# Kernel tuning notes

Hardware: AMD Instinct MI355X
Metric: run time of the kernel (lower is better)

## Reference

```python
import jax, jax.numpy as jnp
import numpy as np

N = 100_000   # nodes
E = 3_200_000 # edges
F = 512       # input features
H = 64        # hidden
C = 64        # classes
K = 10        # APPNP propagation steps
ALPHA = 0.1


def setup_inputs() -> dict:
    key = jax.random.key(0)
    k0, k1, k2, k3 = jax.random.split(key, 4)
    x = jax.random.normal(k0, (N, F), dtype=jnp.float32)
    W1 = jax.random.normal(k1, (H, F), dtype=jnp.float32) / np.float32(np.sqrt(F))
    b1 = jnp.zeros((H,), dtype=jnp.float32)
    W2 = jax.random.normal(k2, (C, H), dtype=jnp.float32) / np.float32(np.sqrt(H))
    b2 = jnp.zeros((C,), dtype=jnp.float32)
    edge_index = jax.random.randint(k3, (2, E), 0, N, dtype=jnp.int64)
    return {"x": x, "W1": W1, "b1": b1, "W2": W2, "b2": b2, "edge_index": edge_index}


def reference(x, W1, b1, W2, b2, edge_index):
    src = edge_index[0]  # message source (x_j)
    dst = edge_index[1]  # aggregation target
    # GCN normalization with self-loops: deg_i = 1 + sum of incoming edge weights
    deg = jax.ops.segment_sum(jnp.ones((E,), x.dtype), dst, num_segments=N) + 1.0
    dinv = jax.lax.rsqrt(deg)
    norm = dinv[src] * dinv[dst]      # per-edge coefficient
    self_w = dinv * dinv              # self-loop coefficient d_i^{-1}

    # MLP (dropout is identity in eval mode)
    h = jax.nn.relu(x @ W1.T + b1)
    h = h @ W2.T + b2                 # [N, C]

    # APPNP: z <- (1-alpha) * A_hat z + alpha * h, repeated K times
    z = h
    for _ in range(K):
        agg = jax.ops.segment_sum(norm[:, None] * z[src], dst, num_segments=N)
        agg = agg + self_w[:, None] * z
        z = (1.0 - ALPHA) * agg + ALPHA * h

    return jax.nn.log_softmax(z, axis=1)
```

## Files before the change

kernel.cpp:

```cpp
#include <hip/hip_runtime.h>
#include <hip/hip_bf16.h>

#define N_NODES 100000
#define N_EDGES 3200000
#define F_IN    512
#define H_DIM   64
#define C_DIM   64
#define K_STEPS 10
#define ALPHA   0.1f
#define RSTRIDE 96
#define NBINS   256
#define BINW    391
#define SLOTS   16384
#define EPB     4096

typedef __attribute__((ext_vector_type(8))) short bf16x8;
typedef __attribute__((ext_vector_type(4))) float f32x4;

__device__ __forceinline__ float bf2f(ushort u) {
    union { unsigned int i; float f; } c; c.i = ((unsigned int)u) << 16; return c.f;
}
__device__ __forceinline__ ushort f2bf(float f) {
    union { float f; unsigned int i; } c; c.f = f;
    unsigned int lsb = (c.i >> 16) & 1u;
    unsigned int r = c.i + 0x7fffu + lsb;
    return (ushort)(r >> 16);
}
__device__ __forceinline__ uint cvtpk(float a, float b) {
    uint r;
    asm("v_cvt_pk_bf16_f32 %0, %1, %2" : "=v"(r) : "v"(a), "v"(b));
    return r;
}

__global__ __launch_bounds__(256) void binA_kernel(
    const int* __restrict__ src, const int* __restrict__ dst,
    int* __restrict__ gcursor, uint* __restrict__ staging, int e)
{
    __shared__ int cnt[NBINS], sbase[NBINS], loff[NBINS], gbase[NBINS];
    __shared__ int wsum[4];
    __shared__ uint recs[EPB];
    __shared__ uchar binarr[EPB];
    int t = threadIdx.x;
    cnt[t] = 0; loff[t] = 0;
    __syncthreads();

    int blk = blockIdx.x * EPB;
    int nhere = e - blk; nhere = (nhere < EPB) ? nhere : EPB;

    #pragma unroll
    for (int j = 0; j < EPB / 256; ++j) {
        int i = blk + j * 256 + t;
        if (i < e) atomicAdd(&cnt[dst[i] / BINW], 1);
    }
    __syncthreads();

    int lane = t & 63, w = t >> 6;
    int v = cnt[t], incl = v;
    #pragma unroll
    for (int off = 1; off < 64; off <<= 1) {
        int u = __shfl_up(incl, off);
        if (lane >= off) incl += u;
    }
    if (lane == 63) wsum[w] = incl;
    __syncthreads();
    int woff = 0;
    #pragma unroll
    for (int j = 0; j < 4; ++j) woff += (j < w) ? wsum[j] : 0;
    sbase[t] = woff + (incl - v);
    gbase[t] = (v > 0) ? atomicAdd(&gcursor[t], v) : 0;
    __syncthreads();

    #pragma unroll
    for (int j = 0; j < EPB / 256; ++j) {
        int i = blk + j * 256 + t;
        if (i < e) {
            int ss = src[i], dd = dst[i];
            int b = dd / BINW;
            int dl = dd - b * BINW;
            int idx = sbase[b] + atomicAdd(&loff[b], 1);
            recs[idx] = (uint)ss | ((uint)dl << 17);
            binarr[idx] = (uchar)b;
        }
    }
    __syncthreads();

    #pragma unroll
    for (int j = 0; j < EPB / 256; ++j) {
        int idx = j * 256 + t;
        if (idx < nhere) {
            int b = binarr[idx];
            int gp = gbase[b] + (idx - sbase[b]);
            if (gp < SLOTS)
                staging[(size_t)b * SLOTS + gp] = recs[idx];
        }
    }
}

__global__ __launch_bounds__(256) void binB_kernel(
    const int* __restrict__ gcursor, const uint* __restrict__ staging,
    int* __restrict__ deg, float* __restrict__ dinv, float* __restrict__ selfc,
    int* __restrict__ esrc, int n)
{
    __shared__ int dloc[BINW];
    int b = blockIdx.x, t = threadIdx.x;
    for (int i = t; i < BINW; i += 256) dloc[i] = 0;
    __syncthreads();

    int cnt = gcursor[b];
    cnt = (cnt < SLOTS) ? cnt : SLOTS;
    const uint* st = staging + (size_t)b * SLOTS;
    int nb = b * BINW;

    int j = t;
    for (; j + 768 < cnt; j += 1024) {
        uint p0 = st[j], p1 = st[j + 256], p2 = st[j + 512], p3 = st[j + 768];
        int d0 = p0 >> 17, d1 = p1 >> 17, d2 = p2 >> 17, d3 = p3 >> 17;
        int q0 = atomicAdd(&dloc[d0], 1);
        int q1 = atomicAdd(&dloc[d1], 1);
        int q2 = atomicAdd(&dloc[d2], 1);
        int q3 = atomicAdd(&dloc[d3], 1);
        if (q0 < RSTRIDE) esrc[(size_t)(nb + d0) * RSTRIDE + q0] = (int)(p0 & 0x1FFFFu);
        if (q1 < RSTRIDE) esrc[(size_t)(nb + d1) * RSTRIDE + q1] = (int)(p1 & 0x1FFFFu);
        if (q2 < RSTRIDE) esrc[(size_t)(nb + d2) * RSTRIDE + q2] = (int)(p2 & 0x1FFFFu);
        if (q3 < RSTRIDE) esrc[(size_t)(nb + d3) * RSTRIDE + q3] = (int)(p3 & 0x1FFFFu);
    }
    for (; j < cnt; j += 256) {
        uint p = st[j];
        int d = p >> 17;
        int q = atomicAdd(&dloc[d], 1);
        if (q < RSTRIDE) esrc[(size_t)(nb + d) * RSTRIDE + q] = (int)(p & 0x1FFFFu);
    }
    __syncthreads();
    for (int i = t; i < BINW; i += 256) {
        int node = nb + i;
        if (node < n) {
            int dg = dloc[i];
            deg[node] = dg;
            float d = rsqrtf((float)dg + 1.0f);
            dinv[node]  = d;
            selfc[node] = (1.0f - ALPHA) * d * d;
        }
    }
}

__global__ void cvt_w_kernel(const float* __restrict__ W1, const float* __restrict__ W2,
                             ushort* __restrict__ w1bf, ushort* __restrict__ w2bf) {
    int i = blockIdx.x * blockDim.x + threadIdx.x;
    if (i < 64 * 512) w1bf[i] = f2bf(W1[i]);
    if (i < 64 * 64)  w2bf[i] = f2bf(W2[i]);
}

__global__ __launch_bounds__(64, 4) void mlp_mfma_kernel(
    const float* __restrict__ x, const ushort* __restrict__ w1bf, const float* __restrict__ b1,
    const ushort* __restrict__ w2bf, const float* __restrict__ b2, const float* __restrict__ dinv,
    ushort* __restrict__ y0, ushort* __restrict__ g, int n)
{
    __shared__ ushort h1s[4096];
    __shared__ float  b1s[64], b2s[64];

    int t = threadIdx.x;
    b1s[t] = b1[t];
    b2s[t] = b2[t];
    __syncthreads();

    int lr = t & 15;
    int lk = t >> 4;
    int rowbase = blockIdx.x * 64;

    f32x4 acc[4][4] = {};
    for (int kk = 0; kk < 16; ++kk) {
        int k0 = kk * 32 + lk * 8;
        bf16x8 a[4];
        #pragma unroll
        for (int fr = 0; fr < 4; ++fr) {
            int row = rowbase + fr * 16 + lr;
            row = (row < n) ? row : (n - 1);
            const float* p = x + (size_t)row * F_IN + k0;
            f32x4 u0 = __builtin_nontemporal_load(reinterpret_cast<const f32x4*>(p));
            f32x4 u1 = __builtin_nontemporal_load(reinterpret_cast<const f32x4*>(p + 4));
            union { uint u[4]; bf16x8 v; } pk;
            pk.u[0] = cvtpk(u0[0], u0[1]);
            pk.u[1] = cvtpk(u0[2], u0[3]);
            pk.u[2] = cvtpk(u1[0], u1[1]);
            pk.u[3] = cvtpk(u1[2], u1[3]);
            a[fr] = pk.v;
        }
        bf16x8 b[4];
        #pragma unroll
        for (int fc = 0; fc < 4; ++fc) {
            int nn = fc * 16 + lr;
            b[fc] = *reinterpret_cast<const bf16x8*>(w1bf + (size_t)nn * F_IN + k0);
        }
        #pragma unroll
        for (int fr = 0; fr < 4; ++fr)
            #pragma unroll
            for (int fc = 0; fc < 4; ++fc)
                acc[fr][fc] = __builtin_amdgcn_mfma_f32_16x16x32_bf16(a[fr], b[fc], acc[fr][fc], 0, 0, 0);
    }

    #pragma unroll
    for (int fr = 0; fr < 4; ++fr) {
        #pragma unroll
        for (int fc = 0; fc < 4; ++fc) {
            #pragma unroll
            for (int reg = 0; reg < 4; ++reg) {
                float vv = acc[fr][fc][reg] + b1s[fc * 16 + lr];
                vv = fmaxf(vv, 0.f);
                int row = fr * 16 + lk * 4 + reg;
                int col = fc * 16 + lr;
                int byte = row * 128 + col * 2;
                *reinterpret_cast<ushort*>((char*)h1s + (byte ^ ((row & 7) << 4))) = f2bf(vv);
            }
        }
    }
    __syncthreads();

    f32x4 acc2[4][4] = {};
    #pragma unroll
    for (int kk = 0; kk < 2; ++kk) {
        int k0 = kk * 32 + lk * 8;
        bf16x8 a2[4], bb[4];
        #pragma unroll
        for (int fr = 0; fr < 4; ++fr) {
            int row = fr * 16 + lr;
            int byte = row * 128 + k0 * 2;
            a2[fr] = *reinterpret_cast<const bf16x8*>((char*)h1s + (byte ^ ((row & 7) << 4)));
        }
        #pragma unroll
        for (int fc = 0; fc < 4; ++fc) {
            int nn = fc * 16 + lr;
            bb[fc] = *reinterpret_cast<const bf16x8*>(w2bf + (size_t)nn * H_DIM + k0);
        }
        #pragma unroll
        for (int fr = 0; fr < 4; ++fr)
            #pragma unroll
            for (int fc = 0; fc < 4; ++fc)
                acc2[fr][fc] = __builtin_amdgcn_mfma_f32_16x16x32_bf16(a2[fr], bb[fc], acc2[fr][fc], 0, 0, 0);
    }

    #pragma unroll
    for (int fr = 0; fr < 4; ++fr) {
        #pragma unroll
        for (int fc = 0; fc < 4; ++fc) {
            #pragma unroll
            for (int reg = 0; reg < 4; ++reg) {
                int row = rowbase + fr * 16 + lk * 4 + reg;
                int col = fc * 16 + lr;
                if (row < n) {
                    float d = dinv[row];
                    float hv = (acc2[fr][fc][reg] + b2s[col]) * d;
                    size_t o = (size_t)row * 64 + col;
                    y0[o] = f2bf(hv);
                    g[o]  = f2bf(ALPHA * hv);
                }
            }
        }
    }
}

template<bool LAST>
__global__ __launch_bounds__(256) void appnp_step_kernel(
    const int* __restrict__ deg, const int* __restrict__ esrc,
    const float* __restrict__ selfc, const float* __restrict__ dinv,
    const ushort* __restrict__ yin, const ushort* __restrict__ g,
    ushort* __restrict__ yout, float* __restrict__ lsm, int n)
{
    int idx = blockIdx.x * blockDim.x + threadIdx.x;
    int wid = idx >> 6;
    if (wid >= n) return;
    int lane = threadIdx.x & 63;
    int q = lane >> 3;
    int p = lane & 7;
    const uint4* y4 = (const uint4*)yin;
    int cnt = deg[wid];
    cnt = (cnt < RSTRIDE) ? cnt : RSTRIDE;
    int base = wid * RSTRIDE;

    float a0 = 0.f, a1 = 0.f, a2 = 0.f, a3 = 0.f;
    float a4 = 0.f, a5 = 0.f, a6 = 0.f, a7 = 0.f;
    int e = 0;
    for (; e + 31 < cnt; e += 32) {
        int s0 = __builtin_nontemporal_load(&esrc[base + e + q]);
        int s1 = __builtin_nontemporal_load(&esrc[base + e + 8 + q]);
        int s2 = __builtin_nontemporal_load(&esrc[base + e + 16 + q]);
        int s3 = __builtin_nontemporal_load(&esrc[base + e + 24 + q]);
        uint4 v0 = y4[(size_t)s0 * 8 + p];
        uint4 v1 = y4[(size_t)s1 * 8 + p];
        uint4 v2 = y4[(size_t)s2 * 8 + p];
        uint4 v3 = y4[(size_t)s3 * 8 + p];
        a0 += bf2f((ushort)v0.x) + bf2f((ushort)v1.x) + bf2f((ushort)v2.x) + bf2f((ushort)v3.x);
        a1 += bf2f((ushort)(v0.x >> 16)) + bf2f((ushort)(v1.x >> 16)) +
              bf2f((ushort)(v2.x >> 16)) + bf2f((ushort)(v3.x >> 16));
        a2 += bf2f((ushort)v0.y) + bf2f((ushort)v1.y) + bf2f((ushort)v2.y) + bf2f((ushort)v3.y);
        a3 += bf2f((ushort)(v0.y >> 16)) + bf2f((ushort)(v1.y >> 16)) +
              bf2f((ushort)(v2.y >> 16)) + bf2f((ushort)(v3.y >> 16));
        a4 += bf2f((ushort)v0.z) + bf2f((ushort)v1.z) + bf2f((ushort)v2.z) + bf2f((ushort)v3.z);
        a5 += bf2f((ushort)(v0.z >> 16)) + bf2f((ushort)(v1.z >> 16)) +
              bf2f((ushort)(v2.z >> 16)) + bf2f((ushort)(v3.z >> 16));
        a6 += bf2f((ushort)v0.w) + bf2f((ushort)v1.w) + bf2f((ushort)v2.w) + bf2f((ushort)v3.w);
        a7 += bf2f((ushort)(v0.w >> 16)) + bf2f((ushort)(v1.w >> 16)) +
              bf2f((ushort)(v2.w >> 16)) + bf2f((ushort)(v3.w >> 16));
    }
    if (e + 15 < cnt) {
        int s0 = __builtin_nontemporal_load(&esrc[base + e + q]);
        int s1 = __builtin_nontemporal_load(&esrc[base + e + 8 + q]);
        uint4 v0 = y4[(size_t)s0 * 8 + p];
        uint4 v1 = y4[(size_t)s1 * 8 + p];
        a0 += bf2f((ushort)v0.x) + bf2f((ushort)v1.x);
        a1 += bf2f((ushort)(v0.x >> 16)) + bf2f((ushort)(v1.x >> 16));
        a2 += bf2f((ushort)v0.y) + bf2f((ushort)v1.y);
        a3 += bf2f((ushort)(v0.y >> 16)) + bf2f((ushort)(v1.y >> 16));
        a4 += bf2f((ushort)v0.z) + bf2f((ushort)v1.z);
        a5 += bf2f((ushort)(v0.z >> 16)) + bf2f((ushort)(v1.z >> 16));
        a6 += bf2f((ushort)v0.w) + bf2f((ushort)v1.w);
        a7 += bf2f((ushort)(v0.w >> 16)) + bf2f((ushort)(v1.w >> 16));
        e += 16;
    }
    for (; e < cnt; e += 8) {
        bool valid = (e + q) < cnt;
        int s = __builtin_nontemporal_load(&esrc[valid ? (base + e + q) : base]);
        uint4 v = y4[(size_t)s * 8 + p];
        if (valid) {
            a0 += bf2f((ushort)v.x); a1 += bf2f((ushort)(v.x >> 16));
            a2 += bf2f((ushort)v.y); a3 += bf2f((ushort)(v.y >> 16));
            a4 += bf2f((ushort)v.z); a5 += bf2f((ushort)(v.z >> 16));
            a6 += bf2f((ushort)v.w); a7 += bf2f((ushort)(v.w >> 16));
        }
    }
    a0 += __shfl_xor(a0, 8); a0 += __shfl_xor(a0, 16); a0 += __shfl_xor(a0, 32);
    a1 += __shfl_xor(a1, 8); a1 += __shfl_xor(a1, 16); a1 += __shfl_xor(a1, 32);
    a2 += __shfl_xor(a2, 8); a2 += __shfl_xor(a2, 16); a2 += __shfl_xor(a2, 32);
    a3 += __shfl_xor(a3, 8); a3 += __shfl_xor(a3, 16); a3 += __shfl_xor(a3, 32);
    a4 += __shfl_xor(a4, 8); a4 += __shfl_xor(a4, 16); a4 += __shfl_xor(a4, 32);
    a5 += __shfl_xor(a5, 8); a5 += __shfl_xor(a5, 16); a5 += __shfl_xor(a5, 32);
    a6 += __shfl_xor(a6, 8); a6 += __shfl_xor(a6, 16); a6 += __shfl_xor(a6, 32);
    a7 += __shfl_xor(a7, 8); a7 += __shfl_xor(a7, 16); a7 += __shfl_xor(a7, 32);

    size_t o4 = (size_t)wid * 8 + p;
    uint4 ys = y4[o4];
    uint4 gg = ((const uint4*)g)[o4];
    float sc = selfc[wid];
    float yn0 = sc * (a0 + bf2f((ushort)ys.x)) + bf2f((ushort)gg.x);
    float yn1 = sc * (a1 + bf2f((ushort)(ys.x >> 16))) + bf2f((ushort)(gg.x >> 16));
    float yn2 = sc * (a2 + bf2f((ushort)ys.y)) + bf2f((ushort)gg.y);
    float yn3 = sc * (a3 + bf2f((ushort)(ys.y >> 16))) + bf2f((ushort)(gg.y >> 16));
    float yn4 = sc * (a4 + bf2f((ushort)ys.z)) + bf2f((ushort)gg.z);
    float yn5 = sc * (a5 + bf2f((ushort)(ys.z >> 16))) + bf2f((ushort)(gg.z >> 16));
    float yn6 = sc * (a6 + bf2f((ushort)ys.w)) + bf2f((ushort)gg.w);
    float yn7 = sc * (a7 + bf2f((ushort)(ys.w >> 16))) + bf2f((ushort)(gg.w >> 16));

    if (!LAST) {
        if (q == 0) {
            uint4 pk;
            pk.x = cvtpk(yn0, yn1);
            pk.y = cvtpk(yn2, yn3);
            pk.z = cvtpk(yn4, yn5);
            pk.w = cvtpk(yn6, yn7);
            ((uint4*)yout)[o4] = pk;
        }
    } else {
        float di = dinv[wid];
        float z0 = yn0 / di, z1 = yn1 / di, z2 = yn2 / di, z3 = yn3 / di;
        float z4 = yn4 / di, z5 = yn5 / di, z6 = yn6 / di, z7 = yn7 / di;
        float m = fmaxf(fmaxf(fmaxf(z0, z1), fmaxf(z2, z3)),
                        fmaxf(fmaxf(z4, z5), fmaxf(z6, z7)));
        #pragma unroll
        for (int off = 4; off > 0; off >>= 1) m = fmaxf(m, __shfl_xor(m, off));
        float s = expf(z0 - m) + expf(z1 - m) + expf(z2 - m) + expf(z3 - m) +
                  expf(z4 - m) + expf(z5 - m) + expf(z6 - m) + expf(z7 - m);
        #pragma unroll
        for (int off = 4; off > 0; off >>= 1) s += __shfl_xor(s, off);
        float ls = logf(s);
        if (q == 0) {
            float* o = &lsm[(size_t)wid * 64 + 8 * p];
            *reinterpret_cast<float4*>(o)     = make_float4(z0 - m - ls, z1 - m - ls,
                                                            z2 - m - ls, z3 - m - ls);
            *reinterpret_cast<float4*>(o + 4) = make_float4(z4 - m - ls, z5 - m - ls,
                                                            z6 - m - ls, z7 - m - ls);
        }
    }
}

extern "C" void kernel_launch(void* const* d_in, const int* in_sizes, int n_in,
                              void* d_out, int out_size, void* d_ws, size_t ws_size,
                              hipStream_t stream) {
    const float* x  = (const float*)d_in[0];
    const float* W1 = (const float*)d_in[1];
    const float* b1 = (const float*)d_in[2];
    const float* W2 = (const float*)d_in[3];
    const float* b2 = (const float*)d_in[4];
    const int*   ei = (const int*)d_in[5];
    const int* src = ei;
    const int* dst = ei + N_EDGES;
    float* out = (float*)d_out;

    char* ws = (char*)d_ws;
    size_t off = 0;
    auto alloc = [&](size_t bytes) -> void* {
        void* p = ws + off;
        off += (bytes + 255) & ~(size_t)255;
        return p;
    };
    int*    deg     = (int*)   alloc((size_t)N_NODES * 4);
    float*  dinv    = (float*) alloc((size_t)N_NODES * 4);
    float*  selfc   = (float*) alloc((size_t)N_NODES * 4);
    int*    gcursor = (int*)   alloc((size_t)NBINS * 4);
    uint*   staging = (uint*)  alloc((size_t)NBINS * SLOTS * 4);
    int*    esrc    = (int*)   alloc((size_t)N_NODES * RSTRIDE * 4);
    ushort* g       = (ushort*)alloc((size_t)N_NODES * 64 * 2);
    ushort* ya      = (ushort*)alloc((size_t)N_NODES * 64 * 2);
    ushort* yb      = (ushort*)alloc((size_t)N_NODES * 64 * 2);
    ushort* w1bf    = (ushort*)alloc((size_t)H_DIM * F_IN * 2);
    ushort* w2bf    = (ushort*)alloc((size_t)C_DIM * H_DIM * 2);

    hipMemsetAsync(gcursor, 0, (size_t)NBINS * 4, stream);
    binA_kernel<<<(N_EDGES + EPB - 1) / EPB, 256, 0, stream>>>(src, dst, gcursor, staging, N_EDGES);
    binB_kernel<<<NBINS, 256, 0, stream>>>(gcursor, staging, deg, dinv, selfc, esrc, N_NODES);
    cvt_w_kernel<<<(H_DIM * F_IN + 255) / 256, 256, 0, stream>>>(W1, W2, w1bf, w2bf);
    mlp_mfma_kernel<<<(N_NODES + 63) / 64, 64, 0, stream>>>(x, w1bf, b1, w2bf, b2, dinv,
                                                            ya, g, N_NODES);

    const int grid = (N_NODES * 64 + 255) / 256;
    ushort* yin = ya;
    ushort* yout = yb;
    for (int k = 0; k < K_STEPS - 1; ++k) {
        appnp_step_kernel<false><<<grid, 256, 0, stream>>>(
            deg, esrc, selfc, dinv, yin, g, yout, nullptr, N_NODES);
        ushort* tmp = yin; yin = yout; yout = tmp;
    }
    appnp_step_kernel<true><<<grid, 256, 0, stream>>>(
        deg, esrc, selfc, dinv, yin, g, nullptr, out, N_NODES);
}
```

Baseline: 752.0 us.

## Cache edge loads in binA, widen binB blocks, shrink MLP tiles, drop g buffer

binA now loads src and dst once with nontemporal loads and keeps them in registers for the second pass, so edges are not re-read from memory. binB runs 512 threads per bin instead of 256. The MLP kernel uses 32-row tiles with higher occupancy bounds and no longer writes a separate alpha*h buffer. The APPNP steps instead read the initial y0 and scale it by ALPHA, with a third ping-pong buffer so y0 is never overwritten. The aim is to cut memory traffic and raise occupancy, at the cost of more registers in binA and half the per-block reuse of the W1 loads in the MLP.

```diff
diff --git a/kernel.cpp b/kernel.cpp
--- a/kernel.cpp
+++ b/kernel.cpp
@@ -47,10 +47,14 @@
     int blk = blockIdx.x * EPB;
     int nhere = e - blk; nhere = (nhere < EPB) ? nhere : EPB;
 
+    int ssr[16], ddr[16];
     #pragma unroll
     for (int j = 0; j < EPB / 256; ++j) {
         int i = blk + j * 256 + t;
-        if (i < e) atomicAdd(&cnt[dst[i] / BINW], 1);
+        bool v = i < e;
+        ssr[j] = v ? __builtin_nontemporal_load(&src[i]) : -1;
+        ddr[j] = v ? __builtin_nontemporal_load(&dst[i]) : 0;
+        if (v) atomicAdd(&cnt[ddr[j] / BINW], 1);
     }
     __syncthreads();
 
@@ -72,13 +76,11 @@
 
     #pragma unroll
     for (int j = 0; j < EPB / 256; ++j) {
-        int i = blk + j * 256 + t;
-        if (i < e) {
-            int ss = src[i], dd = dst[i];
-            int b = dd / BINW;
-            int dl = dd - b * BINW;
+        if (ssr[j] >= 0) {
+            int b = ddr[j] / BINW;
+            int dl = ddr[j] - b * BINW;
             int idx = sbase[b] + atomicAdd(&loff[b], 1);
-            recs[idx] = (uint)ss | ((uint)dl << 17);
+            recs[idx] = (uint)ssr[j] | ((uint)dl << 17);
             binarr[idx] = (uchar)b;
         }
     }
@@ -96,14 +98,14 @@
     }
 }
 
-__global__ __launch_bounds__(256) void binB_kernel(
+__global__ __launch_bounds__(512) void binB_kernel(
     const int* __restrict__ gcursor, const uint* __restrict__ staging,
     int* __restrict__ deg, float* __restrict__ dinv, float* __restrict__ selfc,
     int* __restrict__ esrc, int n)
 {
     __shared__ int dloc[BINW];
     int b = blockIdx.x, t = threadIdx.x;
-    for (int i = t; i < BINW; i += 256) dloc[i] = 0;
+    for (int i = t; i < BINW; i += 512) dloc[i] = 0;
     __syncthreads();
 
     int cnt = gcursor[b];
@@ -112,8 +114,8 @@
     int nb = b * BINW;
 
     int j = t;
-    for (; j + 768 < cnt; j += 1024) {
-        uint p0 = st[j], p1 = st[j + 256], p2 = st[j + 512], p3 = st[j + 768];
+    for (; j + 1536 < cnt; j += 2048) {
+        uint p0 = st[j], p1 = st[j + 512], p2 = st[j + 1024], p3 = st[j + 1536];
         int d0 = p0 >> 17, d1 = p1 >> 17, d2 = p2 >> 17, d3 = p3 >> 17;
         int q0 = atomicAdd(&dloc[d0], 1);
         int q1 = atomicAdd(&dloc[d1], 1);
@@ -124,14 +126,14 @@
         if (q2 < RSTRIDE) esrc[(size_t)(nb + d2) * RSTRIDE + q2] = (int)(p2 & 0x1FFFFu);
         if (q3 < RSTRIDE) esrc[(size_t)(nb + d3) * RSTRIDE + q3] = (int)(p3 & 0x1FFFFu);
     }
-    for (; j < cnt; j += 256) {
+    for (; j < cnt; j += 512) {
         uint p = st[j];
         int d = p >> 17;
         int q = atomicAdd(&dloc[d], 1);
         if (q < RSTRIDE) esrc[(size_t)(nb + d) * RSTRIDE + q] = (int)(p & 0x1FFFFu);
     }
     __syncthreads();
-    for (int i = t; i < BINW; i += 256) {
+    for (int i = t; i < BINW; i += 512) {
         int node = nb + i;
         if (node < n) {
             int dg = dloc[i];
@@ -150,12 +152,12 @@
     if (i < 64 * 64)  w2bf[i] = f2bf(W2[i]);
 }
 
-__global__ __launch_bounds__(64, 4) void mlp_mfma_kernel(
+__global__ __launch_bounds__(64, 8) void mlp_mfma_kernel(
     const float* __restrict__ x, const ushort* __restrict__ w1bf, const float* __restrict__ b1,
     const ushort* __restrict__ w2bf, const float* __restrict__ b2, const float* __restrict__ dinv,
-    ushort* __restrict__ y0, ushort* __restrict__ g, int n)
+    ushort* __restrict__ y0, int n)
 {
-    __shared__ ushort h1s[4096];
+    __shared__ ushort h1s[2048];
     __shared__ float  b1s[64], b2s[64];
 
     int t = threadIdx.x;
@@ -165,14 +167,14 @@
 
     int lr = t & 15;
     int lk = t >> 4;
-    int rowbase = blockIdx.x * 64;
-
-    f32x4 acc[4][4] = {};
+    int rowbase = blockIdx.x * 32;
+
+    f32x4 acc[2][4] = {};
     for (int kk = 0; kk < 16; ++kk) {
         int k0 = kk * 32 + lk * 8;
-        bf16x8 a[4];
-        #pragma unroll
-        for (int fr = 0; fr < 4; ++fr) {
+        bf16x8 a[2];
+        #pragma unroll
+        for (int fr = 0; fr < 2; ++fr) {
             int row = rowbase + fr * 16 + lr;
             row = (row < n) ? row : (n - 1);
             const float* p = x + (size_t)row * F_IN + k0;
@@ -192,14 +194,14 @@
             b[fc] = *reinterpret_cast<const bf16x8*>(w1bf + (size_t)nn * F_IN + k0);
         }
         #pragma unroll
-        for (int fr = 0; fr < 4; ++fr)
+        for (int fr = 0; fr < 2; ++fr)
             #pragma unroll
             for (int fc = 0; fc < 4; ++fc)
                 acc[fr][fc] = __builtin_amdgcn_mfma_f32_16x16x32_bf16(a[fr], b[fc], acc[fr][fc], 0, 0, 0);
     }
 
     #pragma unroll
-    for (int fr = 0; fr < 4; ++fr) {
+    for (int fr = 0; fr < 2; ++fr) {
         #pragma unroll
         for (int fc = 0; fc < 4; ++fc) {
             #pragma unroll
@@ -215,13 +217,13 @@
     }
     __syncthreads();
 
-    f32x4 acc2[4][4] = {};
+    f32x4 acc2[2][4] = {};
     #pragma unroll
     for (int kk = 0; kk < 2; ++kk) {
         int k0 = kk * 32 + lk * 8;
-        bf16x8 a2[4], bb[4];
-        #pragma unroll
-        for (int fr = 0; fr < 4; ++fr) {
+        bf16x8 a2[2], bb[4];
+        #pragma unroll
+        for (int fr = 0; fr < 2; ++fr) {
             int row = fr * 16 + lr;
             int byte = row * 128 + k0 * 2;
             a2[fr] = *reinterpret_cast<const bf16x8*>((char*)h1s + (byte ^ ((row & 7) << 4)));
@@ -232,14 +234,14 @@
             bb[fc] = *reinterpret_cast<const bf16x8*>(w2bf + (size_t)nn * H_DIM + k0);
         }
         #pragma unroll
-        for (int fr = 0; fr < 4; ++fr)
+        for (int fr = 0; fr < 2; ++fr)
             #pragma unroll
             for (int fc = 0; fc < 4; ++fc)
                 acc2[fr][fc] = __builtin_amdgcn_mfma_f32_16x16x32_bf16(a2[fr], bb[fc], acc2[fr][fc], 0, 0, 0);
     }
 
     #pragma unroll
-    for (int fr = 0; fr < 4; ++fr) {
+    for (int fr = 0; fr < 2; ++fr) {
         #pragma unroll
         for (int fc = 0; fc < 4; ++fc) {
             #pragma unroll
@@ -247,11 +249,8 @@
                 int row = rowbase + fr * 16 + lk * 4 + reg;
                 int col = fc * 16 + lr;
                 if (row < n) {
-                    float d = dinv[row];
-                    float hv = (acc2[fr][fc][reg] + b2s[col]) * d;
-                    size_t o = (size_t)row * 64 + col;
-                    y0[o] = f2bf(hv);
-                    g[o]  = f2bf(ALPHA * hv);
+                    float hv = (acc2[fr][fc][reg] + b2s[col]) * dinv[row];
+                    y0[(size_t)row * 64 + col] = f2bf(hv);
                 }
             }
         }
@@ -262,7 +261,7 @@
 __global__ __launch_bounds__(256) void appnp_step_kernel(
     const int* __restrict__ deg, const int* __restrict__ esrc,
     const float* __restrict__ selfc, const float* __restrict__ dinv,
-    const ushort* __restrict__ yin, const ushort* __restrict__ g,
+    const ushort* __restrict__ yin, const ushort* __restrict__ y0buf,
     ushort* __restrict__ yout, float* __restrict__ lsm, int n)
 {
     int idx = blockIdx.x * blockDim.x + threadIdx.x;
@@ -338,16 +337,16 @@
 
     size_t o4 = (size_t)wid * 8 + p;
     uint4 ys = y4[o4];
-    uint4 gg = ((const uint4*)g)[o4];
+    uint4 gg = ((const uint4*)y0buf)[o4];
     float sc = selfc[wid];
-    float yn0 = sc * (a0 + bf2f((ushort)ys.x)) + bf2f((ushort)gg.x);
-    float yn1 = sc * (a1 + bf2f((ushort)(ys.x >> 16))) + bf2f((ushort)(gg.x >> 16));
-    float yn2 = sc * (a2 + bf2f((ushort)ys.y)) + bf2f((ushort)gg.y);
-    float yn3 = sc * (a3 + bf2f((ushort)(ys.y >> 16))) + bf2f((ushort)(gg.y >> 16));
-    float yn4 = sc * (a4 + bf2f((ushort)ys.z)) + bf2f((ushort)gg.z);
-    float yn5 = sc * (a5 + bf2f((ushort)(ys.z >> 16))) + bf2f((ushort)(gg.z >> 16));
-    float yn6 = sc * (a6 + bf2f((ushort)ys.w)) + bf2f((ushort)gg.w);
-    float yn7 = sc * (a7 + bf2f((ushort)(ys.w >> 16))) + bf2f((ushort)(gg.w >> 16));
+    float yn0 = sc * (a0 + bf2f((ushort)ys.x)) + ALPHA * bf2f((ushort)gg.x);
+    float yn1 = sc * (a1 + bf2f((ushort)(ys.x >> 16))) + ALPHA * bf2f((ushort)(gg.x >> 16));
+    float yn2 = sc * (a2 + bf2f((ushort)ys.y)) + ALPHA * bf2f((ushort)gg.y);
+    float yn3 = sc * (a3 + bf2f((ushort)(ys.y >> 16))) + ALPHA * bf2f((ushort)(gg.y >> 16));
+    float yn4 = sc * (a4 + bf2f((ushort)ys.z)) + ALPHA * bf2f((ushort)gg.z);
+    float yn5 = sc * (a5 + bf2f((ushort)(ys.z >> 16))) + ALPHA * bf2f((ushort)(gg.z >> 16));
+    float yn6 = sc * (a6 + bf2f((ushort)ys.w)) + ALPHA * bf2f((ushort)gg.w);
+    float yn7 = sc * (a7 + bf2f((ushort)(ys.w >> 16))) + ALPHA * bf2f((ushort)(gg.w >> 16));
 
     if (!LAST) {
         if (q == 0) {
@@ -407,27 +406,28 @@
     int*    gcursor = (int*)   alloc((size_t)NBINS * 4);
     uint*   staging = (uint*)  alloc((size_t)NBINS * SLOTS * 4);
     int*    esrc    = (int*)   alloc((size_t)N_NODES * RSTRIDE * 4);
-    ushort* g       = (ushort*)alloc((size_t)N_NODES * 64 * 2);
-    ushort* ya      = (ushort*)alloc((size_t)N_NODES * 64 * 2);
+    ushort* y0      = (ushort*)alloc((size_t)N_NODES * 64 * 2);
     ushort* yb      = (ushort*)alloc((size_t)N_NODES * 64 * 2);
+    ushort* yc      = (ushort*)alloc((size_t)N_NODES * 64 * 2);
     ushort* w1bf    = (ushort*)alloc((size_t)H_DIM * F_IN * 2);
     ushort* w2bf    = (ushort*)alloc((size_t)C_DIM * H_DIM * 2);
 
     hipMemsetAsync(gcursor, 0, (size_t)NBINS * 4, stream);
     binA_kernel<<<(N_EDGES + EPB - 1) / EPB, 256, 0, stream>>>(src, dst, gcursor, staging, N_EDGES);
-    binB_kernel<<<NBINS, 256, 0, stream>>>(gcursor, staging, deg, dinv, selfc, esrc, N_NODES);
+    binB_kernel<<<NBINS, 512, 0, stream>>>(gcursor, staging, deg, dinv, selfc, esrc, N_NODES);
     cvt_w_kernel<<<(H_DIM * F_IN + 255) / 256, 256, 0, stream>>>(W1, W2, w1bf, w2bf);
-    mlp_mfma_kernel<<<(N_NODES + 63) / 64, 64, 0, stream>>>(x, w1bf, b1, w2bf, b2, dinv,
-                                                            ya, g, N_NODES);
+    mlp_mfma_kernel<<<(N_NODES + 31) / 32, 64, 0, stream>>>(x, w1bf, b1, w2bf, b2, dinv,
+                                                            y0, N_NODES);
 
     const int grid = (N_NODES * 64 + 255) / 256;
-    ushort* yin = ya;
+    const ushort* yin = y0;
     ushort* yout = yb;
     for (int k = 0; k < K_STEPS - 1; ++k) {
         appnp_step_kernel<false><<<grid, 256, 0, stream>>>(
-            deg, esrc, selfc, dinv, yin, g, yout, nullptr, N_NODES);
-        ushort* tmp = yin; yin = yout; yout = tmp;
+            deg, esrc, selfc, dinv, yin, y0, yout, nullptr, N_NODES);
+        yin = yout;
+        yout = (yout == yb) ? yc : yb;
     }
     appnp_step_kernel<true><<<grid, 256, 0, stream>>>(
-        deg, esrc, selfc, dinv, yin, g, nullptr, out, N_NODES);
-}
+        deg, esrc, selfc, dinv, yin, y0, nullptr, out, N_NODES);
+}
```

New measurement: 789.6 us. 5.0% more time.
